# Kernel optimization log

Hardware: AMD Instinct MI355X
Metric: run time of the kernel (lower is better)

The kernel has to match this reference:

```python
import jax, jax.numpy as jnp
import numpy as np

N_MEL = 80; ENC = 512; ARNN = 1024; DRNN = 1024; PRE = 256
ADIM = 128; NFILT = 32; KS = 31
B = 16; T_ENC = 128; T_DEC = 128
NEG = -1e30  # stand-in for -inf mask value


def _lstm_cell(x, h, c, wih, whh, bih, bhh):
    # PyTorch LSTMCell gate order: i, f, g, o
    gates = x @ wih.T + h @ whh.T + bih + bhh
    i, f, g, o = jnp.split(gates, 4, axis=-1)
    c = jax.nn.sigmoid(f) * c + jax.nn.sigmoid(i) * jnp.tanh(g)
    h = jax.nn.sigmoid(o) * jnp.tanh(c)
    return h, c


def _forward(memory, mels, memory_lengths, prenet_w1, prenet_w2,
             arnn_wih, arnn_whh, arnn_bih, arnn_bhh,
             query_w, memory_w, v_w, loc_conv_w, loc_dense_w,
             drnn_wih, drnn_whh, drnn_bih, drnn_bhh,
             proj_w, proj_b, gate_w, gate_b):
    bsz, t_enc, enc = memory.shape
    t_dec = mels.shape[2]
    valid = jnp.arange(t_enc)[None, :] < memory_lengths[:, None]  # [B,T_enc]
    proc_mem = memory @ memory_w.T  # [B,T_enc,ADIM], precomputed once

    # parse_decoder_inputs + go frame: use go frame + teacher frames 0..T-2
    teacher = jnp.transpose(mels, (2, 0, 1))  # [T_dec,B,n_mel]
    go = jnp.zeros((1, bsz, mels.shape[1]), mels.dtype)
    dec_in = jnp.concatenate([go, teacher], axis=0)[:t_dec]
    # Prenet (dropout is p=0.0 in source, so omitted)
    x = jax.nn.relu(dec_in @ prenet_w1.T)
    x = jax.nn.relu(x @ prenet_w2.T)  # [T_dec,B,PRE]

    pad = (KS - 1) // 2

    def step(carry, x_t):
        attn_h, attn_c, dec_h, dec_c, aw, awc, ctx = carry
        # attention RNN
        cell_in = jnp.concatenate([x_t, ctx], axis=-1)
        attn_h2, attn_c2 = _lstm_cell(cell_in, attn_h, attn_c,
                                      arnn_wih, arnn_whh, arnn_bih, arnn_bhh)
        # location-sensitive attention
        aw_cat = jnp.stack([aw, awc], axis=1)  # [B,2,T_enc]
        loc = jax.lax.conv_general_dilated(
            aw_cat, loc_conv_w, (1,), [(pad, pad)],
            dimension_numbers=('NCH', 'OIH', 'NCH'))  # [B,NFILT,T_enc]
        loc = jnp.einsum('bft,af->bta', loc, loc_dense_w)  # [B,T_enc,ADIM]
        pq = attn_h2 @ query_w.T  # [B,ADIM]
        e = jnp.tanh(pq[:, None, :] + loc + proc_mem) @ v_w[0]  # [B,T_enc]
        e = jnp.where(valid, e, NEG)
        aw2 = jax.nn.softmax(e, axis=1)
        ctx2 = jnp.einsum('bt,bte->be', aw2, memory)  # [B,ENC]
        awc2 = awc + aw2
        # decoder RNN
        dec_in2 = jnp.concatenate([attn_h2, ctx2], axis=-1)
        dec_h2, dec_c2 = _lstm_cell(dec_in2, dec_h, dec_c,
                                    drnn_wih, drnn_whh, drnn_bih, drnn_bhh)
        hc = jnp.concatenate([dec_h2, ctx2], axis=-1)
        mel = hc @ proj_w.T + proj_b      # [B,n_mel]
        gate = hc @ gate_w.T + gate_b     # [B,1]
        new_carry = (attn_h2, attn_c2, dec_h2, dec_c2, aw2, awc2, ctx2)
        return new_carry, (mel, gate[:, 0], aw2)

    z = lambda *s: jnp.zeros(s, memory.dtype)
    carry0 = (z(bsz, ARNN), z(bsz, ARNN), z(bsz, DRNN), z(bsz, DRNN),
              z(bsz, t_enc), z(bsz, t_enc), z(bsz, enc))
    _, (mels_out, gates, aligns) = jax.lax.scan(step, carry0, x)
    mel_outputs = jnp.transpose(mels_out, (1, 2, 0))   # [B,n_mel,T_dec]
    gate_outputs = jnp.transpose(gates, (1, 0))        # [B,T_dec]
    alignments = jnp.transpose(aligns, (1, 0, 2))      # [B,T_dec,T_enc]
    return mel_outputs, gate_outputs, alignments


def setup_inputs() -> dict:
    key = jax.random.key(0)
    ks = jax.random.split(key, 24)

    def g(i, shape):
        fan_in = shape[-1] if len(shape) <= 2 else int(np.prod(shape[1:]))
        return jax.random.normal(ks[i], shape, jnp.float32) / np.float32(np.sqrt(fan_in))

    return {
        'memory': jax.random.normal(ks[0], (B, T_ENC, ENC), jnp.float32),
        'mels': jax.random.normal(ks[1], (B, N_MEL, T_DEC), jnp.float32),
        'memory_lengths': jax.random.randint(ks[2], (B,), T_ENC // 2, T_ENC + 1),
        'prenet_w1': g(3, (PRE, N_MEL)),
        'prenet_w2': g(4, (PRE, PRE)),
        'arnn_wih': g(5, (4 * ARNN, PRE + ENC)),
        'arnn_whh': g(6, (4 * ARNN, ARNN)),
        'arnn_bih': g(7, (4 * ARNN,)),
        'arnn_bhh': g(8, (4 * ARNN,)),
        'query_w': g(9, (ADIM, ARNN)),
        'memory_w': g(10, (ADIM, ENC)),
        'v_w': g(11, (1, ADIM)),
        'loc_conv_w': g(12, (NFILT, 2, KS)),
        'loc_dense_w': g(13, (ADIM, NFILT)),
        'drnn_wih': g(14, (4 * DRNN, ARNN + ENC)),
        'drnn_whh': g(15, (4 * DRNN, DRNN)),
        'drnn_bih': g(16, (4 * DRNN,)),
        'drnn_bhh': g(17, (4 * DRNN,)),
        'proj_w': g(18, (N_MEL, DRNN + ENC)),
        'proj_b': g(19, (N_MEL,)),
        'gate_w': g(20, (1, DRNN + ENC)),
        'gate_b': g(21, (1,)),
    }


def reference(memory, mels, memory_lengths, prenet_w1, prenet_w2,
              arnn_wih, arnn_whh, arnn_bih, arnn_bhh,
              query_w, memory_w, v_w, loc_conv_w, loc_dense_w,
              drnn_wih, drnn_whh, drnn_bih, drnn_bhh,
              proj_w, proj_b, gate_w, gate_b):
    return _forward(memory, mels, memory_lengths, prenet_w1, prenet_w2,
                    arnn_wih, arnn_whh, arnn_bih, arnn_bhh,
                    query_w, memory_w, v_w, loc_conv_w, loc_dense_w,
                    drnn_wih, drnn_whh, drnn_bih, drnn_bhh,
                    proj_w, proj_b, gate_w, gate_b)
```

## Files before the change

kernel.cpp:

```cpp
#include <hip/hip_runtime.h>
#include <hip/hip_cooperative_groups.h>

namespace cg = cooperative_groups;

#define N_MEL 80
#define ENC   512
#define ARNN  1024
#define PRE   256
#define ADIM  128
#define NFILT 32
#define KS    31
#define BSZ   16
#define TENC  128
#define TDEC  128

#define OFF_XA     0u
#define OFF_X      8388608u
#define OFF_H1     8912896u
#define OFF_DECIN  9437184u
#define OFF_PM     9601024u
#define OFF_ATTNH  9863168u
#define OFF_DECH   9895936u
#define OFF_CTX    9928704u
#define OFF_CTR    9945088u
#define STATE_FLOATS 83520

typedef float vf4 __attribute__((ext_vector_type(4)));

__device__ __forceinline__ float sigmf(float x) { return 1.0f / (1.0f + __expf(-x)); }
__device__ __forceinline__ float tanhfast(float x) { return 1.0f - 2.0f / (__expf(2.0f * x) + 1.0f); }
__device__ __forceinline__ float dot4(const float4& w, const vf4& x) {
    return w.x * x.x + w.y * x.y + w.z * x.z + w.w * x.w;
}
__device__ __forceinline__ float dot4f(const float4& w, const float4& x) {
    return w.x * x.x + w.y * x.y + w.z * x.z + w.w * x.w;
}

__device__ __forceinline__ vf4 vload4(const float* p) { return *(const volatile vf4*)p; }
__device__ __forceinline__ float vloadf(const float* p) { return *(const volatile float*)p; }
__device__ __forceinline__ void vstoref(float* p, float v) { *(volatile float*)p = v; }

__device__ __forceinline__ void wait_ge(unsigned* p, unsigned tgt) {
    while (__hip_atomic_load(p, __ATOMIC_RELAXED, __HIP_MEMORY_SCOPE_AGENT) < tgt)
        __builtin_amdgcn_s_sleep(1);
    asm volatile("" ::: "memory");
}

#define LDS_SPIN(idx, tgt)                                                      \
    do {                                                                        \
        float j0_ = 1.f, j1_ = 1.f;                                             \
        while (__hip_atomic_load(&s_done[idx], __ATOMIC_RELAXED,                \
                                 __HIP_MEMORY_SCOPE_WORKGROUP) < (tgt)) {       \
            _Pragma("unroll")                                                   \
            for (int i_ = 0; i_ < 32; i_++) {                                   \
                j0_ = __builtin_fmaf(j0_, 1.0000001f, 1e-30f);                  \
                j1_ = __builtin_fmaf(j1_, 0.9999999f, 1e-30f);                  \
            }                                                                   \
        }                                                                       \
        asm volatile("" :: "v"(j0_), "v"(j1_));                                 \
        asm volatile("" ::: "memory");                                          \
    } while (0)

#define LDS_POST(idx, val)                                                      \
    __hip_atomic_store(&s_done[idx], (int)(val), __ATOMIC_RELAXED,              \
                       __HIP_MEMORY_SCOPE_WORKGROUP)


__global__ void __launch_bounds__(1024) build_decin(const float* __restrict__ mels,
                                                    float* __restrict__ decin) {
    int idx = blockIdx.x * 1024 + threadIdx.x;
    if (idx >= 128 * 16 * 80) return;
    int t = idx / 1280, r = idx % 1280;
    int b = r / 80, m = r % 80;
    decin[idx] = (t == 0) ? 0.f : mels[b * (80 * 128) + m * 128 + (t - 1)];
}

__global__ void __launch_bounds__(256) gemm_kernel(
    const float* __restrict__ A, int lda,
    const float* __restrict__ B, int ldb,
    float* __restrict__ C, int ldc,
    int M, int N, int K,
    const float* __restrict__ bias1, const float* __restrict__ bias2, int relu) {
    __shared__ float As[16][68];
    __shared__ float Bs[16][68];
    int tid = threadIdx.x;
    int tn = tid & 15, tm = tid >> 4;
    int m0 = blockIdx.y * 64, n0 = blockIdx.x * 64;
    float acc[4][4] = {};
    for (int k0 = 0; k0 < K; k0 += 16) {
        for (int idx = tid; idx < 1024; idx += 256) {
            int mm = idx >> 4, kk = idx & 15;
            int kg = k0 + kk;
            As[kk][mm] = (kg < K) ? A[(size_t)(m0 + mm) * lda + kg] : 0.f;
            Bs[kk][mm] = (kg < K) ? B[(size_t)(n0 + mm) * ldb + kg] : 0.f;
        }
        __syncthreads();
#pragma unroll
        for (int kk = 0; kk < 16; kk++) {
            float av[4], bv[4];
#pragma unroll
            for (int i = 0; i < 4; i++) { av[i] = As[kk][tm * 4 + i]; bv[i] = Bs[kk][tn * 4 + i]; }
#pragma unroll
            for (int i = 0; i < 4; i++)
#pragma unroll
                for (int j = 0; j < 4; j++) acc[i][j] += av[i] * bv[j];
        }
        __syncthreads();
    }
    for (int i = 0; i < 4; i++) {
        int m = m0 + tm * 4 + i;
        for (int j = 0; j < 4; j++) {
            int n = n0 + tn * 4 + j;
            float v = acc[i][j];
            if (bias1) v += bias1[n];
            if (bias2) v += bias2[n];
            if (relu) v = fmaxf(v, 0.f);
            C[(size_t)m * ldc + n] = v;
        }
    }
}


struct DecArgs {
    const float* memory;
    const int* memlen;
    const float* arnn_wih;
    const float* arnn_whh;
    const float* drnn_wih;
    const float* drnn_whh;
    const float* drnn_bih;
    const float* drnn_bhh;
    const float* query_w;
    const float* v_w;
    const float* conv_w;
    const float* dense_w;
    const float* proj_w;
    const float* proj_b;
    const float* gate_w;
    const float* gate_b;
    float* ws;
    float* out;
};

__global__ void __launch_bounds__(512, 2) decoder_main(DecArgs A) {
    cg::grid_group grid = cg::this_grid();
    const int tid = threadIdx.x;
    const int wv = tid >> 6;
    const int l = tid & 63;
    const int blk = blockIdx.x;
    const int u = wv & 3;
    const int kq = wv >> 2;
    const int jj = blk * 4 + u;
    const int col = kq * 256 + l * 4;
    float* ws = A.ws;
    unsigned* ctrA = (unsigned*)(ws + OFF_CTR);
    unsigned* ctrB = (unsigned*)(ws + OFF_CTR + 32);
    const int grp = blk >> 4;
    unsigned* subA   = (unsigned*)(ws + OFF_CTR + 64 + grp * 32);
    unsigned* bcastA = (unsigned*)(ws + OFF_CTR + 576);
    unsigned* bcastB = (unsigned*)(ws + OFF_CTR + 1088);

    __shared__ float s_pm[128 * 132];
    __shared__ float s_loc[128 * 33];
    __shared__ float s_dw[128 * 33];
    __shared__ float s_cw[1984];
    __shared__ float s_ah[1024];
    __shared__ float s_ep[512];
    __shared__ float s_part[8][64];
    __shared__ float s_pp[8][64];
    __shared__ float s_pq[128];
    __shared__ float s_aw2[128];
    __shared__ float s_awl[128];
    __shared__ float s_awcl[128];
    __shared__ float s_attnc[64];
    __shared__ float s_decc[64];
    __shared__ float s_db[16];
    __shared__ float s_vw[128];
    __shared__ float s_red[2];
    __shared__ int   s_done[2];

    {
        int g = blk * 512 + tid;
        if (g < STATE_FLOATS) ws[OFF_ATTNH + g] = 0.f;
    }
    if (tid < 2) s_done[tid] = 0;
    if (tid < 128) { s_awl[tid] = 0.f; s_awcl[tid] = 0.f; }
    if (tid < 64) { s_attnc[tid] = 0.f; s_decc[tid] = 0.f; }
    if (tid < 16) {
        int uu = tid >> 2, gg = tid & 3;
        s_db[tid] = A.drnn_bih[gg * 1024 + blk * 4 + uu] + A.drnn_bhh[gg * 1024 + blk * 4 + uu];
    }
    if (tid < 128) s_vw[tid] = A.v_w[tid];
    for (int idx = tid; idx < 4096; idx += 512) {
        int a = idx >> 5, f = idx & 31;
        s_dw[a * 33 + f] = A.dense_w[idx];
    }
    if (blk < 16) {
        for (int idx = tid; idx < 16384; idx += 512) {
            int tt = idx >> 7, a = idx & 127;
            s_pm[tt * 132 + a] = ws[OFF_PM + (blk * 128 + tt) * 128 + a];
        }
        for (int idx = tid; idx < 1984; idx += 512) s_cw[idx] = A.conv_w[idx];
    }
    const int ml = (blk < 16) ? A.memlen[blk] : 0;

    float4 wA[12];
    {
#pragma unroll
        for (int g = 0; g < 4; g++)
            wA[g] = *reinterpret_cast<const float4*>(
                A.arnn_wih + (size_t)(g * 1024 + jj) * 768 + 256 + col);
#pragma unroll
        for (int ch = 1; ch < 3; ch++)
#pragma unroll
            for (int g = 0; g < 4; g++)
                wA[ch * 4 + g] = *reinterpret_cast<const float4*>(
                    A.arnn_whh + (size_t)(g * 1024 + jj) * 1024 + (ch - 1) * 512 + col);
    }
    float4 wD[20];
    {
#pragma unroll
        for (int ch = 0; ch < 3; ch++)
#pragma unroll
            for (int g = 0; g < 4; g++)
                wD[ch * 4 + g] = *reinterpret_cast<const float4*>(
                    A.drnn_wih + (size_t)(g * 1024 + jj) * 1536 + ch * 512 + col);
#pragma unroll
        for (int ch = 3; ch < 5; ch++)
#pragma unroll
            for (int g = 0; g < 4; g++)
                wD[ch * 4 + g] = *reinterpret_cast<const float4*>(
                    A.drnn_whh + (size_t)(g * 1024 + jj) * 1024 + (ch - 3) * 512 + col);
    }
    __syncthreads();
    grid.sync();

    auto reduce4 = [&](float p0, float p1, float p2, float p3) -> float {
        float a01 = (l & 1) ? p1 : p0;
        float b01 = (l & 1) ? p0 : p1;
        a01 += __shfl_xor(b01, 1);
        float a23 = (l & 1) ? p3 : p2;
        float b23 = (l & 1) ? p2 : p3;
        a23 += __shfl_xor(b23, 1);
        float k_ = (l & 2) ? a23 : a01;
        float s_ = (l & 2) ? a01 : a23;
        k_ += __shfl_xor(s_, 2);
        k_ += __shfl_xor(k_, 4);
        k_ += __shfl_xor(k_, 8);
        k_ += __shfl_xor(k_, 16);
        k_ += __shfl_xor(k_, 32);
        return k_;
    };

    auto attn_stage = [&](int t, int wpar, int rpar) {
        const float* hb = ws + OFF_ATTNH + rpar * 16384;
        const float* cb = ws + OFF_CTX + rpar * 8192;
        float xa0 = 0.f, xa1 = 0.f, xa2 = 0.f, xa3 = 0.f;
        if (tid < 64) {
            int eb = tid & 15, eu = tid >> 4;
            const float* xa = ws + OFF_XA + (size_t)(t * 16 + eb) * 4096 + (blk * 4 + eu);
            xa0 = xa[0]; xa1 = xa[1024]; xa2 = xa[2048]; xa3 = xa[3072];
        }
#pragma unroll 4
        for (int b = 0; b < 16; b++) {
            vf4 x0 = vload4(cb + b * 512 + col);
            vf4 x1 = vload4(hb + b * 1024 + col);
            vf4 x2 = vload4(hb + b * 1024 + 512 + col);
            float p0 = dot4(wA[0], x0) + dot4(wA[4], x1) + dot4(wA[8], x2);
            float p1 = dot4(wA[1], x0) + dot4(wA[5], x1) + dot4(wA[9], x2);
            float p2 = dot4(wA[2], x0) + dot4(wA[6], x1) + dot4(wA[10], x2);
            float p3 = dot4(wA[3], x0) + dot4(wA[7], x1) + dot4(wA[11], x2);
            float r = reduce4(p0, p1, p2, p3);
            if (l < 4) s_part[wv][b * 4 + l] = r;
        }
        __syncthreads();
        if (tid < 64) {
            int eu = tid >> 4, eb = tid & 15;
            float G0 = s_part[eu][eb * 4 + 0] + s_part[eu + 4][eb * 4 + 0] + xa0;
            float G1 = s_part[eu][eb * 4 + 1] + s_part[eu + 4][eb * 4 + 1] + xa1;
            float G2 = s_part[eu][eb * 4 + 2] + s_part[eu + 4][eb * 4 + 2] + xa2;
            float G3 = s_part[eu][eb * 4 + 3] + s_part[eu + 4][eb * 4 + 3] + xa3;
            float ig = sigmf(G0), fg = sigmf(G1), gg = tanhfast(G2), og = sigmf(G3);
            float c = fg * s_attnc[tid] + ig * gg;
            s_attnc[tid] = c;
            vstoref(ws + OFF_ATTNH + wpar * 16384 + eb * 1024 + blk * 4 + eu, og * tanhfast(c));
        }
    };

    auto dec_partial = [&](int wpar, int rpar) {
        const float* hb = ws + OFF_ATTNH + wpar * 16384;
        const float* db = ws + OFF_DECH + rpar * 16384;
#pragma unroll 2
        for (int b = 0; b < 16; b++) {
            vf4 x0 = vload4(hb + b * 1024 + col);
            vf4 x1 = vload4(hb + b * 1024 + 512 + col);
            vf4 x3 = vload4(db + b * 1024 + col);
            vf4 x4 = vload4(db + b * 1024 + 512 + col);
            float p0 = dot4(wD[0], x0) + dot4(wD[4], x1) + dot4(wD[12], x3) + dot4(wD[16], x4);
            float p1 = dot4(wD[1], x0) + dot4(wD[5], x1) + dot4(wD[13], x3) + dot4(wD[17], x4);
            float p2 = dot4(wD[2], x0) + dot4(wD[6], x1) + dot4(wD[14], x3) + dot4(wD[18], x4);
            float p3 = dot4(wD[3], x0) + dot4(wD[7], x1) + dot4(wD[15], x3) + dot4(wD[19], x4);
            float r = reduce4(p0, p1, p2, p3);
            if (l < 4) s_pp[wv][b * 4 + l] = r;
        }
    };

    auto dec_tail = [&](int wpar) {
        const float* cb = ws + OFF_CTX + wpar * 8192;
#pragma unroll 4
        for (int b = 0; b < 16; b++) {
            vf4 x2 = vload4(cb + b * 512 + col);
            float p0 = dot4(wD[8], x2);
            float p1 = dot4(wD[9], x2);
            float p2 = dot4(wD[10], x2);
            float p3 = dot4(wD[11], x2);
            float r = reduce4(p0, p1, p2, p3);
            if (l < 4) s_part[wv][b * 4 + l] = r;
        }
        __syncthreads();
        if (tid < 64) {
            int eu = tid >> 4, eb = tid & 15;
            float G0 = s_part[eu][eb * 4 + 0] + s_part[eu + 4][eb * 4 + 0]
                     + s_pp[eu][eb * 4 + 0] + s_pp[eu + 4][eb * 4 + 0] + s_db[eu * 4 + 0];
            float G1 = s_part[eu][eb * 4 + 1] + s_part[eu + 4][eb * 4 + 1]
                     + s_pp[eu][eb * 4 + 1] + s_pp[eu + 4][eb * 4 + 1] + s_db[eu * 4 + 1];
            float G2 = s_part[eu][eb * 4 + 2] + s_part[eu + 4][eb * 4 + 2]
                     + s_pp[eu][eb * 4 + 2] + s_pp[eu + 4][eb * 4 + 2] + s_db[eu * 4 + 2];
            float G3 = s_part[eu][eb * 4 + 3] + s_part[eu + 4][eb * 4 + 3]
                     + s_pp[eu][eb * 4 + 3] + s_pp[eu + 4][eb * 4 + 3] + s_db[eu * 4 + 3];
            float ig = sigmf(G0), fg = sigmf(G1), gg = tanhfast(G2), og = sigmf(G3);
            float c = fg * s_decc[tid] + ig * gg;
            s_decc[tid] = c;
            vstoref(ws + OFF_DECH + wpar * 16384 + eb * 1024 + blk * 4 + eu, og * tanhfast(c));
        }
        __syncthreads();
    };

    auto loc_conv = [&]() {
        for (int idx = tid; idx < 4096; idx += 512) {
            int f = idx >> 7, tt = idx & 127;
            const float* w0 = s_cw + f * 62;
            float s = 0.f;
#pragma unroll
            for (int k = 0; k < 31; k++) {
                int j = tt + k - 15;
                if (j >= 0 && j < 128) s += w0[k] * s_awl[j] + w0[31 + k] * s_awcl[j];
            }
            s_loc[tt * 33 + f] = s;
        }
    };

    auto attention_rest = [&](int t, int wpar) {
        const int b = blk;
        s_ah[tid] = vloadf(ws + OFF_ATTNH + wpar * 16384 + b * 1024 + tid);
        s_ah[tid + 512] = vloadf(ws + OFF_ATTNH + wpar * 16384 + b * 1024 + 512 + tid);
        __syncthreads();
#pragma unroll 4
        for (int ii = 0; ii < 16; ii++) {
            int a = wv * 16 + ii;
            const float* qw = A.query_w + a * 1024;
            float s = 0.f;
#pragma unroll
            for (int q = 0; q < 4; q++) {
                int k = q * 256 + l * 4;
                float4 h4 = *reinterpret_cast<const float4*>(&s_ah[k]);
                float4 w4 = *reinterpret_cast<const float4*>(&qw[k]);
                s += dot4f(w4, h4);
            }
#pragma unroll
            for (int off = 1; off < 64; off <<= 1) s += __shfl_xor(s, off);
            if (l == 0) s_pq[a] = s;
        }
        __syncthreads();
        {
            int tt = tid >> 2, sl = tid & 3;
            float part = 0.f;
            for (int i = 0; i < 32; i++) {
                int a = i * 4 + sl;
                float lp = 0.f;
#pragma unroll
                for (int f = 0; f < 32; f++) lp += s_loc[tt * 33 + f] * s_dw[a * 33 + f];
                float arg = s_pq[a] + lp + s_pm[tt * 132 + a];
                part += s_vw[a] * tanhfast(arg);
            }
            s_ep[tid] = part;
        }
        __syncthreads();
        if (tid < 128) {
            float s = s_ep[tid * 4] + s_ep[tid * 4 + 1] + s_ep[tid * 4 + 2] + s_ep[tid * 4 + 3];
            s_aw2[tid] = (tid >= ml) ? 0.f : __expf(s);
        }
        __syncthreads();
        if (wv == 0) {
            float s = s_aw2[l] + s_aw2[l + 64];
#pragma unroll
            for (int off = 1; off < 64; off <<= 1) s += __shfl_xor(s, off);
            if (l == 0) s_red[0] = 1.f / s;
        }
        __syncthreads();
        if (tid < 128) {
            float val = s_aw2[tid] * s_red[0];
            s_aw2[tid] = val;
            s_awl[tid] = val;
            s_awcl[tid] += val;
            A.out[165888 + b * 16384 + t * 128 + tid] = val;
        }
        __syncthreads();
        {
            const float* mb = A.memory + (size_t)b * 65536 + tid;
            float acc = 0.f;
#pragma unroll 8
            for (int tt2 = 0; tt2 < 128; tt2++) acc += s_aw2[tt2] * mb[tt2 * 512];
            vstoref(ws + OFF_CTX + wpar * 8192 + b * 512 + tid, acc);
        }
    };

    auto eout = [&](int tdone) {
        int widx = (blk - 16) * 8 + wv;
        if (widx >= 1296) return;
        int ppar = tdone & 1;
        int b; const float* wrow; float bias; float* dst;
        if (widx < 1280) {
            b = widx / 80; int m = widx % 80;
            wrow = A.proj_w + m * 1536; bias = A.proj_b[m];
            dst = A.out + (size_t)(b * 80 + m) * 128 + tdone;
        } else {
            b = widx - 1280;
            wrow = A.gate_w; bias = A.gate_b[0];
            dst = A.out + 163840 + b * 128 + tdone;
        }
        const float* h1p = ws + OFF_DECH + ppar * 16384 + b * 1024;
        const float* c1p = ws + OFF_CTX + ppar * 8192 + b * 512;
        float s = 0.f;
#pragma unroll
        for (int q = 0; q < 6; q++) {
            int k = q * 256 + l * 4;
            float4 w4 = *reinterpret_cast<const float4*>(&wrow[k]);
            vf4 h4;
            if (k < 1024) h4 = vload4(h1p + k);
            else h4 = vload4(c1p + k - 1024);
            s += dot4(w4, h4);
        }
#pragma unroll
        for (int off = 1; off < 64; off <<= 1) s += __shfl_xor(s, off);
        if (l == 0) *dst = s + bias;
    };

    for (int t = 0; t < 128; t++) {
        int wpar = t & 1, rpar = wpar ^ 1;
        unsigned tg = (unsigned)(t + 1);
        attn_stage(t, wpar, rpar);
        __syncthreads();
        if (tid == 0) {
            asm volatile("s_waitcnt vmcnt(0)" ::: "memory");
            unsigned old = __hip_atomic_fetch_add(subA, 1u, __ATOMIC_RELAXED,
                                                  __HIP_MEMORY_SCOPE_AGENT);
            if (old == 16u * tg - 1u)
                __hip_atomic_fetch_add(ctrA, 1u, __ATOMIC_RELAXED,
                                       __HIP_MEMORY_SCOPE_AGENT);
        }
        if (blk < 16) {
            loc_conv();
            __syncthreads();
            if (tid == 0) {
                wait_ge(ctrA, 16u * tg);
                __hip_atomic_store(bcastA + blk * 8, tg, __ATOMIC_RELAXED,
                                   __HIP_MEMORY_SCOPE_AGENT);
                LDS_POST(0, tg);
            } else if (wv > 0) LDS_SPIN(0, (int)tg);
            __syncthreads();
            attention_rest(t, wpar);
            __syncthreads();
            if (tid == 0) {
                asm volatile("s_waitcnt vmcnt(0)" ::: "memory");
                __hip_atomic_fetch_add(ctrB, 1u, __ATOMIC_RELAXED,
                                       __HIP_MEMORY_SCOPE_AGENT);
            }
            dec_partial(wpar, rpar);
            if (tid == 0) {
                wait_ge(ctrB, 16u * tg);
                __hip_atomic_store(bcastB + blk * 8, tg, __ATOMIC_RELAXED,
                                   __HIP_MEMORY_SCOPE_AGENT);
                LDS_POST(1, tg);
            } else if (wv > 0) LDS_SPIN(1, (int)tg);
            __syncthreads();
            dec_tail(wpar);
        } else {
            if (tid == 0) {
                wait_ge(bcastA + grp * 8, tg);
                LDS_POST(0, tg);
            } else if (wv > 0) LDS_SPIN(0, (int)tg);
            __syncthreads();
            if (t >= 1) eout(t - 1);
            dec_partial(wpar, rpar);
            if (tid == 0) {
                wait_ge(bcastB + grp * 8, tg);
                LDS_POST(1, tg);
            } else if (wv > 0) LDS_SPIN(1, (int)tg);
            __syncthreads();
            dec_tail(wpar);
        }
    }
    if (tid == 0) {
        asm volatile("s_waitcnt vmcnt(0)" ::: "memory");
        unsigned old = __hip_atomic_fetch_add(subA, 1u, __ATOMIC_RELAXED,
                                              __HIP_MEMORY_SCOPE_AGENT);
        if (old == 16u * 129u - 1u)
            __hip_atomic_fetch_add(ctrA, 1u, __ATOMIC_RELAXED, __HIP_MEMORY_SCOPE_AGENT);
    }
    if (blk < 16) {
        if (tid == 0) {
            wait_ge(ctrA, 16u * 129u);
            __hip_atomic_store(bcastA + blk * 8, 129u, __ATOMIC_RELAXED,
                               __HIP_MEMORY_SCOPE_AGENT);
        }
    } else {
        if (tid == 0) { wait_ge(bcastA + grp * 8, 129u); LDS_POST(0, 129); }
        else if (wv > 0) LDS_SPIN(0, 129);
        __syncthreads();
        eout(127);
    }
}


extern "C" void kernel_launch(void* const* d_in, const int* in_sizes, int n_in,
                              void* d_out, int out_size, void* d_ws, size_t ws_size,
                              hipStream_t stream) {
    (void)in_sizes; (void)n_in; (void)out_size; (void)ws_size;
    const float* memory    = (const float*)d_in[0];
    const float* mels      = (const float*)d_in[1];
    const int*   memlen    = (const int*)d_in[2];
    const float* prenet_w1 = (const float*)d_in[3];
    const float* prenet_w2 = (const float*)d_in[4];
    const float* arnn_wih  = (const float*)d_in[5];
    const float* arnn_whh  = (const float*)d_in[6];
    const float* arnn_bih  = (const float*)d_in[7];
    const float* arnn_bhh  = (const float*)d_in[8];
    const float* query_w   = (const float*)d_in[9];
    const float* memory_w  = (const float*)d_in[10];
    const float* v_w       = (const float*)d_in[11];
    const float* conv_w    = (const float*)d_in[12];
    const float* dense_w   = (const float*)d_in[13];
    const float* drnn_wih  = (const float*)d_in[14];
    const float* drnn_whh  = (const float*)d_in[15];
    const float* drnn_bih  = (const float*)d_in[16];
    const float* drnn_bhh  = (const float*)d_in[17];
    const float* proj_w    = (const float*)d_in[18];
    const float* proj_b    = (const float*)d_in[19];
    const float* gate_w    = (const float*)d_in[20];
    const float* gate_b    = (const float*)d_in[21];
    float* ws = (float*)d_ws;
    float* out = (float*)d_out;

    build_decin<<<dim3(160), dim3(1024), 0, stream>>>(mels, ws + OFF_DECIN);
    gemm_kernel<<<dim3(4, 32), dim3(256), 0, stream>>>(ws + OFF_DECIN, 80, prenet_w1, 80,
                                                       ws + OFF_H1, 256, 2048, 256, 80,
                                                       nullptr, nullptr, 1);
    gemm_kernel<<<dim3(4, 32), dim3(256), 0, stream>>>(ws + OFF_H1, 256, prenet_w2, 256,
                                                       ws + OFF_X, 256, 2048, 256, 256,
                                                       nullptr, nullptr, 1);
    gemm_kernel<<<dim3(64, 32), dim3(256), 0, stream>>>(ws + OFF_X, 256, arnn_wih, 768,
                                                        ws + OFF_XA, 4096, 2048, 4096, 256,
                                                        arnn_bih, arnn_bhh, 0);
    gemm_kernel<<<dim3(2, 32), dim3(256), 0, stream>>>(memory, 512, memory_w, 512,
                                                       ws + OFF_PM, 128, 2048, 128, 512,
                                                       nullptr, nullptr, 0);

    DecArgs a;
    a.memory = memory; a.memlen = memlen;
    a.arnn_wih = arnn_wih; a.arnn_whh = arnn_whh;
    a.drnn_wih = drnn_wih; a.drnn_whh = drnn_whh;
    a.drnn_bih = drnn_bih; a.drnn_bhh = drnn_bhh;
    a.query_w = query_w; a.v_w = v_w;
    a.conv_w = conv_w; a.dense_w = dense_w;
    a.proj_w = proj_w; a.proj_b = proj_b;
    a.gate_w = gate_w; a.gate_b = gate_b;
    a.ws = ws; a.out = out;
    void* kargs[] = { &a };
    hipLaunchCooperativeKernel((const void*)decoder_main, dim3(256), dim3(512),
                               kargs, 0, stream);
}
```

Before: 11.94 ms.

## Stage shared hidden-state vectors in LDS before matvec reductions

The attention-LSTM, decoder-LSTM partial, decoder tail and output-projection stages now cooperatively copy the global hidden/context vectors into a new 32KB shared staging buffer with vectorized volatile loads, then read them from LDS. Previously every wave issued its own volatile global loads for the same vectors. The spin-wait on LDS flags also switches from an FMA busy loop to s_sleep. The change adds extra __syncthreads per chunk and raises LDS use, which may lower occupancy given launch_bounds(512,2) and already large shared arrays. The s_sleep may also add wake-up latency on the intra-block critical path.

```diff
diff --git a/kernel.cpp b/kernel.cpp
--- a/kernel.cpp
+++ b/kernel.cpp
@@ -37,7 +37,6 @@
 }
 
 __device__ __forceinline__ vf4 vload4(const float* p) { return *(const volatile vf4*)p; }
-__device__ __forceinline__ float vloadf(const float* p) { return *(const volatile float*)p; }
 __device__ __forceinline__ void vstoref(float* p, float v) { *(volatile float*)p = v; }
 
 __device__ __forceinline__ void wait_ge(unsigned* p, unsigned tgt) {
@@ -48,16 +47,9 @@
 
 #define LDS_SPIN(idx, tgt)                                                      \
     do {                                                                        \
-        float j0_ = 1.f, j1_ = 1.f;                                             \
         while (__hip_atomic_load(&s_done[idx], __ATOMIC_RELAXED,                \
-                                 __HIP_MEMORY_SCOPE_WORKGROUP) < (tgt)) {       \
-            _Pragma("unroll")                                                   \
-            for (int i_ = 0; i_ < 32; i_++) {                                   \
-                j0_ = __builtin_fmaf(j0_, 1.0000001f, 1e-30f);                  \
-                j1_ = __builtin_fmaf(j1_, 0.9999999f, 1e-30f);                  \
-            }                                                                   \
-        }                                                                       \
-        asm volatile("" :: "v"(j0_), "v"(j1_));                                 \
+                                 __HIP_MEMORY_SCOPE_WORKGROUP) < (tgt))         \
+            __builtin_amdgcn_s_sleep(1);                                        \
         asm volatile("" ::: "memory");                                          \
     } while (0)
 
@@ -160,6 +152,7 @@
     unsigned* bcastA = (unsigned*)(ws + OFF_CTR + 576);
     unsigned* bcastB = (unsigned*)(ws + OFF_CTR + 1088);
 
+    __shared__ float s_stg[8192];
     __shared__ float s_pm[128 * 132];
     __shared__ float s_loc[128 * 33];
     __shared__ float s_dw[128 * 33];
@@ -261,19 +254,35 @@
             const float* xa = ws + OFF_XA + (size_t)(t * 16 + eb) * 4096 + (blk * 4 + eu);
             xa0 = xa[0]; xa1 = xa[1024]; xa2 = xa[2048]; xa3 = xa[3072];
         }
-#pragma unroll 4
-        for (int b = 0; b < 16; b++) {
-            vf4 x0 = vload4(cb + b * 512 + col);
-            vf4 x1 = vload4(hb + b * 1024 + col);
-            vf4 x2 = vload4(hb + b * 1024 + 512 + col);
-            float p0 = dot4(wA[0], x0) + dot4(wA[4], x1) + dot4(wA[8], x2);
-            float p1 = dot4(wA[1], x0) + dot4(wA[5], x1) + dot4(wA[9], x2);
-            float p2 = dot4(wA[2], x0) + dot4(wA[6], x1) + dot4(wA[10], x2);
-            float p3 = dot4(wA[3], x0) + dot4(wA[7], x1) + dot4(wA[11], x2);
-            float r = reduce4(p0, p1, p2, p3);
-            if (l < 4) s_part[wv][b * 4 + l] = r;
-        }
-        __syncthreads();
+        for (int c = 0; c < 4; c++) {
+            {
+                int bl = tid >> 7, r = (tid & 127) << 2;
+                *(vf4*)(s_stg + bl * 1536 + r) = vload4(cb + (c * 4 + bl) * 512 + r);
+#pragma unroll
+                for (int k = 0; k < 2; k++) {
+                    int e = tid + k * 512;
+                    int bl2 = e >> 8, r2 = (e & 255) << 2;
+                    *(vf4*)(s_stg + bl2 * 1536 + 512 + r2) =
+                        vload4(hb + (c * 4 + bl2) * 1024 + r2);
+                }
+            }
+            __syncthreads();
+#pragma unroll
+            for (int bl = 0; bl < 4; bl++) {
+                int b = c * 4 + bl;
+                const float* sb = s_stg + bl * 1536;
+                float4 x0 = *(const float4*)(sb + col);
+                float4 x1 = *(const float4*)(sb + 512 + col);
+                float4 x2 = *(const float4*)(sb + 1024 + col);
+                float p0 = dot4f(wA[0], x0) + dot4f(wA[4], x1) + dot4f(wA[8], x2);
+                float p1 = dot4f(wA[1], x0) + dot4f(wA[5], x1) + dot4f(wA[9], x2);
+                float p2 = dot4f(wA[2], x0) + dot4f(wA[6], x1) + dot4f(wA[10], x2);
+                float p3 = dot4f(wA[3], x0) + dot4f(wA[7], x1) + dot4f(wA[11], x2);
+                float r = reduce4(p0, p1, p2, p3);
+                if (l < 4) s_part[wv][b * 4 + l] = r;
+            }
+            __syncthreads();
+        }
         if (tid < 64) {
             int eu = tid >> 4, eb = tid & 15;
             float G0 = s_part[eu][eb * 4 + 0] + s_part[eu + 4][eb * 4 + 0] + xa0;
@@ -288,32 +297,52 @@
     };
 
     auto dec_partial = [&](int wpar, int rpar) {
-        const float* hb = ws + OFF_ATTNH + wpar * 16384;
-        const float* db = ws + OFF_DECH + rpar * 16384;
-#pragma unroll 2
-        for (int b = 0; b < 16; b++) {
-            vf4 x0 = vload4(hb + b * 1024 + col);
-            vf4 x1 = vload4(hb + b * 1024 + 512 + col);
-            vf4 x3 = vload4(db + b * 1024 + col);
-            vf4 x4 = vload4(db + b * 1024 + 512 + col);
-            float p0 = dot4(wD[0], x0) + dot4(wD[4], x1) + dot4(wD[12], x3) + dot4(wD[16], x4);
-            float p1 = dot4(wD[1], x0) + dot4(wD[5], x1) + dot4(wD[13], x3) + dot4(wD[17], x4);
-            float p2 = dot4(wD[2], x0) + dot4(wD[6], x1) + dot4(wD[14], x3) + dot4(wD[18], x4);
-            float p3 = dot4(wD[3], x0) + dot4(wD[7], x1) + dot4(wD[15], x3) + dot4(wD[19], x4);
-            float r = reduce4(p0, p1, p2, p3);
-            if (l < 4) s_pp[wv][b * 4 + l] = r;
+        const float* ha = ws + OFF_ATTNH + wpar * 16384;
+        const float* hd = ws + OFF_DECH + rpar * 16384;
+        for (int c = 0; c < 4; c++) {
+#pragma unroll
+            for (int k = 0; k < 2; k++) {
+                int e = tid + k * 512;
+                int bl = e >> 8, r = (e & 255) << 2;
+                *(vf4*)(s_stg + bl * 2048 + r)        = vload4(ha + (c * 4 + bl) * 1024 + r);
+                *(vf4*)(s_stg + bl * 2048 + 1024 + r) = vload4(hd + (c * 4 + bl) * 1024 + r);
+            }
+            __syncthreads();
+#pragma unroll
+            for (int bl = 0; bl < 4; bl++) {
+                int b = c * 4 + bl;
+                const float* sb = s_stg + bl * 2048;
+                float4 x0 = *(const float4*)(sb + col);
+                float4 x1 = *(const float4*)(sb + 512 + col);
+                float4 x3 = *(const float4*)(sb + 1024 + col);
+                float4 x4 = *(const float4*)(sb + 1536 + col);
+                float p0 = dot4f(wD[0], x0) + dot4f(wD[4], x1) + dot4f(wD[12], x3) + dot4f(wD[16], x4);
+                float p1 = dot4f(wD[1], x0) + dot4f(wD[5], x1) + dot4f(wD[13], x3) + dot4f(wD[17], x4);
+                float p2 = dot4f(wD[2], x0) + dot4f(wD[6], x1) + dot4f(wD[14], x3) + dot4f(wD[18], x4);
+                float p3 = dot4f(wD[3], x0) + dot4f(wD[7], x1) + dot4f(wD[15], x3) + dot4f(wD[19], x4);
+                float r = reduce4(p0, p1, p2, p3);
+                if (l < 4) s_pp[wv][b * 4 + l] = r;
+            }
+            __syncthreads();
         }
     };
 
     auto dec_tail = [&](int wpar) {
-        const float* cb = ws + OFF_CTX + wpar * 8192;
+        const float* cw = ws + OFF_CTX + wpar * 8192;
+#pragma unroll
+        for (int k = 0; k < 4; k++) {
+            int e = tid + k * 512;
+            int bl = e >> 7, r = (e & 127) << 2;
+            *(vf4*)(s_stg + bl * 512 + r) = vload4(cw + bl * 512 + r);
+        }
+        __syncthreads();
 #pragma unroll 4
         for (int b = 0; b < 16; b++) {
-            vf4 x2 = vload4(cb + b * 512 + col);
-            float p0 = dot4(wD[8], x2);
-            float p1 = dot4(wD[9], x2);
-            float p2 = dot4(wD[10], x2);
-            float p3 = dot4(wD[11], x2);
+            float4 x2 = *(const float4*)(s_stg + b * 512 + col);
+            float p0 = dot4f(wD[8], x2);
+            float p1 = dot4f(wD[9], x2);
+            float p2 = dot4f(wD[10], x2);
+            float p3 = dot4f(wD[11], x2);
             float r = reduce4(p0, p1, p2, p3);
             if (l < 4) s_part[wv][b * 4 + l] = r;
         }
@@ -352,8 +381,9 @@
 
     auto attention_rest = [&](int t, int wpar) {
         const int b = blk;
-        s_ah[tid] = vloadf(ws + OFF_ATTNH + wpar * 16384 + b * 1024 + tid);
-        s_ah[tid + 512] = vloadf(ws + OFF_ATTNH + wpar * 16384 + b * 1024 + 512 + tid);
+        if (tid < 256)
+            *(vf4*)(s_ah + tid * 4) =
+                vload4(ws + OFF_ATTNH + wpar * 16384 + b * 1024 + tid * 4);
         __syncthreads();
 #pragma unroll 4
         for (int ii = 0; ii < 16; ii++) {
@@ -416,34 +446,54 @@
     };
 
     auto eout = [&](int tdone) {
-        int widx = (blk - 16) * 8 + wv;
-        if (widx >= 1296) return;
+        int wbase = (blk - 16) * 8;
         int ppar = tdone & 1;
-        int b; const float* wrow; float bias; float* dst;
-        if (widx < 1280) {
-            b = widx / 80; int m = widx % 80;
-            wrow = A.proj_w + m * 1536; bias = A.proj_b[m];
-            dst = A.out + (size_t)(b * 80 + m) * 128 + tdone;
-        } else {
-            b = widx - 1280;
-            wrow = A.gate_w; bias = A.gate_b[0];
-            dst = A.out + 163840 + b * 128 + tdone;
-        }
-        const float* h1p = ws + OFF_DECH + ppar * 16384 + b * 1024;
-        const float* c1p = ws + OFF_CTX + ppar * 8192 + b * 512;
-        float s = 0.f;
-#pragma unroll
-        for (int q = 0; q < 6; q++) {
-            int k = q * 256 + l * 4;
-            float4 w4 = *reinterpret_cast<const float4*>(&wrow[k]);
-            vf4 h4;
-            if (k < 1024) h4 = vload4(h1p + k);
-            else h4 = vload4(c1p + k - 1024);
-            s += dot4(w4, h4);
-        }
-#pragma unroll
-        for (int off = 1; off < 64; off <<= 1) s += __shfl_xor(s, off);
-        if (l == 0) *dst = s + bias;
+        const float* hdp = ws + OFF_DECH + ppar * 16384;
+        const float* cxp = ws + OFF_CTX + ppar * 8192;
+        int b0 = -1;
+        if (wbase < 1280) {
+            b0 = wbase / 80;
+            if (tid < 384) {
+                int rf = tid << 2;
+                vf4 v = (rf < 1024) ? vload4(hdp + b0 * 1024 + rf)
+                                    : vload4(cxp + b0 * 512 + (rf - 1024));
+                *(vf4*)(s_stg + rf) = v;
+            }
+        }
+        __syncthreads();
+        int widx = wbase + wv;
+        if (widx < 1296) {
+            if (widx < 1280) {
+                int m = widx % 80;
+                const float* wrow = A.proj_w + m * 1536;
+                float s = 0.f;
+#pragma unroll
+                for (int q = 0; q < 6; q++) {
+                    int k = q * 256 + l * 4;
+                    float4 w4 = *reinterpret_cast<const float4*>(&wrow[k]);
+                    float4 h4 = *(const float4*)(s_stg + k);
+                    s += dot4f(w4, h4);
+                }
+#pragma unroll
+                for (int off = 1; off < 64; off <<= 1) s += __shfl_xor(s, off);
+                if (l == 0) A.out[(size_t)(b0 * 80 + m) * 128 + tdone] = s + A.proj_b[m];
+            } else {
+                int b = widx - 1280;
+                float s = 0.f;
+#pragma unroll
+                for (int q = 0; q < 6; q++) {
+                    int k = q * 256 + l * 4;
+                    float4 w4 = *reinterpret_cast<const float4*>(&A.gate_w[k]);
+                    vf4 h4 = (k < 1024) ? vload4(hdp + b * 1024 + k)
+                                        : vload4(cxp + b * 512 + k - 1024);
+                    s += dot4(w4, h4);
+                }
+#pragma unroll
+                for (int off = 1; off < 64; off <<= 1) s += __shfl_xor(s, off);
+                if (l == 0) A.out[163840 + b * 128 + tdone] = s + A.gate_b[0];
+            }
+        }
+        __syncthreads();
     };
 
     for (int t = 0; t < 128; t++) {
```

Measured after the change: 11.26 ms. -5.7%, faster.
